# Kernel tuning notes

Measured on AMD Instinct MI355X. Metric: run time of the kernel, lower is better.

## Reference

```python
import math
import jax, jax.numpy as jnp
import numpy as np

N_HEAD = 16
STEP_DIM = 4


def _make_mask(T):
    # lower-triangular causal mask with every STEP_DIM-th column zeroed
    m = jnp.tril(jnp.ones((T, T), dtype=jnp.float32))
    cols = jnp.arange(T)
    keep_col = (cols % STEP_DIM) != (STEP_DIM - 1)
    return m * keep_col[None, :].astype(jnp.float32)  # [T, T]


def setup_inputs() -> dict:
    key = jax.random.key(0)
    ks = jax.random.split(key, 9)
    B, T, C = 2, 2048, 1024
    s = 1.0 / math.sqrt(C)
    return {
        "x": jax.random.normal(ks[0], (B, T, C), dtype=jnp.float32),
        "Wq": jax.random.normal(ks[1], (C, C), dtype=jnp.float32) * s,
        "bq": jnp.zeros((C,), dtype=jnp.float32),
        "Wk": jax.random.normal(ks[2], (C, C), dtype=jnp.float32) * s,
        "bk": jnp.zeros((C,), dtype=jnp.float32),
        "Wv": jax.random.normal(ks[3], (C, C), dtype=jnp.float32) * s,
        "bv": jnp.zeros((C,), dtype=jnp.float32),
        "Wp": jax.random.normal(ks[4], (C, C), dtype=jnp.float32) * s,
        "bp": jnp.zeros((C,), dtype=jnp.float32),
    }


def reference(x, Wq, bq, Wk, bk, Wv, bv, Wp, bp):
    B, T, C = x.shape
    H = N_HEAD
    D = C // H
    # QKV projections -> [B, H, T, D]
    def heads(y):
        return y.reshape(B, T, H, D).transpose(0, 2, 1, 3)
    q = heads(x @ Wq + bq)
    k = heads(x @ Wk + bk)
    v = heads(x @ Wv + bv)
    # scores [B, H, T, T]
    att = jnp.einsum("bhtd,bhsd->bhts", q, k) * (1.0 / math.sqrt(D))
    mask = _make_mask(T)  # [T, T]
    att = jnp.where(mask[None, None, :, :] == 0, -jnp.inf, att)
    att = jax.nn.softmax(att, axis=-1)
    y = jnp.einsum("bhts,bhsd->bhtd", att, v)  # [B, H, T, D]
    y = y.transpose(0, 2, 1, 3).reshape(B, T, C)
    return y @ Wp + bp
```

## Files before the change

kernel.cpp:

```cpp
#include <hip/hip_runtime.h>

typedef __bf16 bf16x8 __attribute__((ext_vector_type(8)));
typedef float  f32x4  __attribute__((ext_vector_type(4)));
typedef unsigned int u32x2 __attribute__((ext_vector_type(2)));
typedef __attribute__((address_space(3))) const unsigned short* lds_cp;

#define T_SEQ 2048
#define C_DIM 1024
#define NH    16
#define HD    64
#define LOG2E 1.4426950408889634f

__device__ __forceinline__ unsigned short f2bf(float f) {
  unsigned u = __builtin_bit_cast(unsigned, f);
  u += 0x7FFFu + ((u >> 16) & 1u);
  return (unsigned short)(u >> 16);
}

__device__ __forceinline__ unsigned cvtpk(float lo, float hi) {
  unsigned r;
  asm("v_cvt_pk_bf16_f32 %0, %1, %2" : "=v"(r) : "v"(lo), "v"(hi));
  return r;
}

__device__ __forceinline__ bf16x8 tr_frag(lds_cp addr) {
  u32x2 lo, hi;
  asm volatile("ds_read_b64_tr_b16 %0, %2 offset:0\n\t"
               "ds_read_b64_tr_b16 %1, %2 offset:128"
               : "=&v"(lo), "=&v"(hi) : "v"(addr) : "memory");
  struct { u32x2 a, b; } s{lo, hi};
  return __builtin_bit_cast(bf16x8, s);
}

__device__ __forceinline__ void gload_lds16(const void* g, void* l) {
  __builtin_amdgcn_global_load_lds(
      (const __attribute__((address_space(1))) unsigned int*)g,
      (__attribute__((address_space(3))) unsigned int*)l, 16, 0, 0);
}

__global__ void k_cvt_x(const float* __restrict__ x, unsigned short* __restrict__ xb) {
  const int i = blockIdx.x * 256 + threadIdx.x;
  const float4 v = ((const float4*)x)[i];
  ushort4 o;
  o.x = f2bf(v.x); o.y = f2bf(v.y); o.z = f2bf(v.z); o.w = f2bf(v.w);
  ((ushort4*)xb)[i] = o;
}

__global__ void k_transpose_w(const float* __restrict__ W, unsigned short* __restrict__ Wt) {
  __shared__ float tile[32][33];
  const int tx = threadIdx.x, ty = threadIdx.y;
  const int n0 = blockIdx.x * 32, k0 = blockIdx.y * 32;
#pragma unroll
  for (int i = 0; i < 32; i += 8)
    tile[ty + i][tx] = W[(size_t)(k0 + ty + i) * C_DIM + n0 + tx];
  __syncthreads();
#pragma unroll
  for (int i = 0; i < 32; i += 8)
    Wt[(size_t)(n0 + ty + i) * C_DIM + k0 + tx] = f2bf(tile[tx][ty + i]);
}

__global__ void k_concat_bias(const float* __restrict__ bq, const float* __restrict__ bk,
                              const float* __restrict__ bv, float* __restrict__ o) {
  const int i = blockIdx.x * 256 + threadIdx.x;
  o[i] = (i < 1024) ? bq[i] : (i < 2048 ? bk[i - 1024] : bv[i - 2048]);
}

template<int KDIM>
__device__ __forceinline__ void gemm_tile_mainloop(
    const unsigned short* __restrict__ A,
    const unsigned short* __restrict__ Bt,
    int m0, int n0,
    unsigned short* As, unsigned short* Bs,
    f32x4 acc[4][4])
{
  const int tid  = threadIdx.x;
  const int lane = tid & 63;
  const int wave = tid >> 6;
  const int wr   = wave >> 1, wc = wave & 1;
  const int srow = lane >> 2;
  const int scol = (lane & 3) << 3;
  const int fr   = lane & 15, g = lane >> 4;

  const f32x4 zero = {0.f, 0.f, 0.f, 0.f};
#pragma unroll
  for (int m = 0; m < 4; ++m)
#pragma unroll
    for (int n = 0; n < 4; ++n) acc[m][n] = zero;

  const int nk = KDIM >> 5;
  for (int kt = 0; kt < nk; ++kt) {
    const int kb = kt << 5;
#pragma unroll
    for (int i = 0; i < 2; ++i) {
      const int c   = wave * 2 + i;
      const int row = c * 16 + srow;
      gload_lds16(A  + (size_t)(m0 + row) * KDIM + kb + scol, As + c * 512);
      gload_lds16(Bt + (size_t)(n0 + row) * KDIM + kb + scol, Bs + c * 512);
    }
    __syncthreads();
    bf16x8 af[4], bfr[4];
    const unsigned short* ap = As + (wr * 64 + fr) * 32 + g * 8;
    const unsigned short* bp = Bs + (wc * 64 + fr) * 32 + g * 8;
#pragma unroll
    for (int m = 0; m < 4; ++m) af[m]  = *(const bf16x8*)(ap + m * 512);
#pragma unroll
    for (int n = 0; n < 4; ++n) bfr[n] = *(const bf16x8*)(bp + n * 512);
#pragma unroll
    for (int m = 0; m < 4; ++m)
#pragma unroll
      for (int n = 0; n < 4; ++n)
        acc[m][n] = __builtin_amdgcn_mfma_f32_16x16x32_bf16(af[m], bfr[n], acc[m][n], 0, 0, 0);
    __syncthreads();
  }
}

__global__ __launch_bounds__(256) void k_gemm_qkv(
    const unsigned short* __restrict__ Xb,
    const unsigned short* __restrict__ Wt,
    const float* __restrict__ bias,
    unsigned short* __restrict__ Qb,
    unsigned short* __restrict__ Kb,
    unsigned short* __restrict__ Vt)
{
  __shared__ __attribute__((aligned(16))) unsigned short As[128 * 32];
  __shared__ __attribute__((aligned(16))) unsigned short Bs[128 * 32];
  f32x4 acc[4][4];
  const int m0 = blockIdx.y * 128, n0 = blockIdx.x * 128;
  gemm_tile_mainloop<1024>(Xb, Wt, m0, n0, As, Bs, acc);

  const int lane = threadIdx.x & 63, wave = threadIdx.x >> 6;
  const int wr = wave >> 1, wc = wave & 1;
  const int fr = lane & 15, g = lane >> 4;
  const int j = n0 >> 10;
#pragma unroll
  for (int ni = 0; ni < 4; ++ni) {
    const int col = n0 + wc * 64 + ni * 16 + fr;
    const int c = col & 1023, h = c >> 6, d = c & 63;
    const float bb = bias[col];
#pragma unroll
    for (int mi = 0; mi < 4; ++mi)
#pragma unroll
      for (int r = 0; r < 4; ++r) {
        const int row = m0 + wr * 64 + mi * 16 + g * 4 + r;
        const int b = row >> 11, t = row & 2047;
        const int bh = b * NH + h;
        const float v = acc[mi][ni][r] + bb;
        if (j == 0)      Qb[((size_t)bh * T_SEQ + t) * HD + d] = f2bf(v * (0.125f * LOG2E));
        else if (j == 1) Kb[((size_t)bh * T_SEQ + t) * HD + d] = f2bf(v);
        else             Vt[((size_t)bh * HD + d) * T_SEQ + t] = f2bf(v);
      }
  }
}

__global__ __launch_bounds__(128) void k_attn(
    const unsigned short* __restrict__ Qb,
    const unsigned short* __restrict__ Kb,
    const unsigned short* __restrict__ Vt,
    unsigned short* __restrict__ Yb)
{
  __shared__ __attribute__((aligned(128))) unsigned short Ks[2][64][64];
  __shared__ __attribute__((aligned(128))) unsigned short Vs[2][64][64];
  __shared__ __attribute__((aligned(128))) unsigned short Pc[2][2][64][16];

  const int i    = blockIdx.x;
  const int xcd  = i & 7;
  const int jj   = i >> 3;
  const int bh   = xcd * 4 + (jj & 3);
  const int qtile = 31 - (jj >> 2);
  const int lane  = threadIdx.x & 63;
  const int wave  = threadIdx.x >> 6;
  const int fr = lane & 15, g = lane >> 4;
  const int q0w = qtile * 64 + wave * 32;
  const int nt = qtile + 1;
  const size_t hbase = (size_t)bh * T_SEQ * HD;
  const unsigned short* Kh = Kb + hbase;
  const unsigned short* Vh = Vt + (size_t)bh * HD * T_SEQ;

  const int srow = lane >> 3;
  const int scol = ((lane & 7) ^ srow) << 3;
  const int frx  = (fr & 7) << 3;

  const unsigned short* qp = Qb + hbase + (size_t)(q0w + fr) * HD + g * 8;
  const bf16x8 qA0 = *(const bf16x8*)(qp);
  const bf16x8 qA1 = *(const bf16x8*)(qp + 32);
  const bf16x8 qB0 = *(const bf16x8*)(qp + 16 * HD);
  const bf16x8 qB1 = *(const bf16x8*)(qp + 16 * HD + 32);

  const f32x4 zero = {0.f, 0.f, 0.f, 0.f};
  f32x4 yA[4], yB[4];
#pragma unroll
  for (int n = 0; n < 4; ++n) { yA[n] = zero; yB[n] = zero; }
  float lA[4], lB[4];
#pragma unroll
  for (int r = 0; r < 4; ++r) { lA[r] = 0.f; lB[r] = 0.f; }
  const float colmul = ((fr & 3) != 3) ? 1.0f : 0.0f;

  char* pwA = (char*)&Pc[wave][0][0][0] + fr * 32 + g * 8;
  char* pwB = (char*)&Pc[wave][1][0][0] + fr * 32 + g * 8;
  lds_cp trA = (lds_cp)(const unsigned short*)&Pc[wave][0][0][0] + fr * 4 + g * 128;
  lds_cp trB = (lds_cp)(const unsigned short*)&Pc[wave][1][0][0] + fr * 4 + g * 128;

  auto STAGE = [&](int buf, int s0) {
#pragma unroll
    for (int i2 = 0; i2 < 4; ++i2) {
      const int c = wave * 4 + i2;
      gload_lds16(Kh + (size_t)(s0 + c * 8 + srow) * HD + scol, &Ks[buf][c * 8][0]);
      gload_lds16(Vh + (size_t)(c * 8 + srow) * T_SEQ + s0 + scol, &Vs[buf][c * 8][0]);
    }
  };

  auto BODY = [&](int cur, int s0, bool diag) {
    bf16x8 kf[4][2];
#pragma unroll
    for (int n = 0; n < 4; ++n) {
      const unsigned short* kr = &Ks[cur][n * 16 + fr][0];
      kf[n][0] = *(const bf16x8*)(kr + ((g * 8) ^ frx));
      kf[n][1] = *(const bf16x8*)(kr + ((32 + g * 8) ^ frx));
    }
    f32x4 sA[4], sB[4];
#pragma unroll
    for (int n = 0; n < 4; ++n) {
      f32x4 a = zero, b = zero;
      a = __builtin_amdgcn_mfma_f32_16x16x32_bf16(qA0, kf[n][0], a, 0, 0, 0);
      a = __builtin_amdgcn_mfma_f32_16x16x32_bf16(qA1, kf[n][1], a, 0, 0, 0);
      b = __builtin_amdgcn_mfma_f32_16x16x32_bf16(qB0, kf[n][0], b, 0, 0, 0);
      b = __builtin_amdgcn_mfma_f32_16x16x32_bf16(qB1, kf[n][1], b, 0, 0, 0);
      sA[n] = a; sB[n] = b;
    }
    if (diag) {
      const bool colok = (fr & 3) != 3;
#pragma unroll
      for (int n = 0; n < 4; ++n) {
        const int sc = s0 + n * 16 + fr;
#pragma unroll
        for (int r = 0; r < 4; ++r) {
          const int tA = q0w + g * 4 + r;
          sA[n][r] = (colok && sc <= tA) ? sA[n][r] : -1e30f;
          sB[n][r] = (colok && sc <= tA + 16) ? sB[n][r] : -1e30f;
        }
      }
    }
    bf16x8 vf[4][2];
#pragma unroll
    for (int n = 0; n < 4; ++n) {
      const unsigned short* vr = &Vs[cur][n * 16 + fr][0];
      vf[n][0] = *(const bf16x8*)(vr + ((g * 8) ^ frx));
      vf[n][1] = *(const bf16x8*)(vr + ((32 + g * 8) ^ frx));
    }
#pragma unroll
    for (int n = 0; n < 4; ++n) {
      float pa0 = exp2f(sA[n][0]), pa1 = exp2f(sA[n][1]);
      float pa2 = exp2f(sA[n][2]), pa3 = exp2f(sA[n][3]);
      float pb0 = exp2f(sB[n][0]), pb1 = exp2f(sB[n][1]);
      float pb2 = exp2f(sB[n][2]), pb3 = exp2f(sB[n][3]);
      if (!diag) {
        pa0 *= colmul; pa1 *= colmul; pa2 *= colmul; pa3 *= colmul;
        pb0 *= colmul; pb1 *= colmul; pb2 *= colmul; pb3 *= colmul;
      }
      lA[0] += pa0; lA[1] += pa1; lA[2] += pa2; lA[3] += pa3;
      lB[0] += pb0; lB[1] += pb1; lB[2] += pb2; lB[3] += pb3;
      u32x2 wa = {cvtpk(pa0, pa1), cvtpk(pa2, pa3)};
      u32x2 wb = {cvtpk(pb0, pb1), cvtpk(pb2, pb3)};
      *(u32x2*)(pwA + n * 512) = wa;
      *(u32x2*)(pwB + n * 512) = wb;
    }
    bf16x8 paA[2], paB[2];
    paA[0] = tr_frag(trA);       paA[1] = tr_frag(trA + 512);
    paB[0] = tr_frag(trB);       paB[1] = tr_frag(trB + 512);
    asm volatile("s_waitcnt lgkmcnt(0)" ::: "memory");
    __builtin_amdgcn_sched_barrier(0);
#pragma unroll
    for (int kk = 0; kk < 2; ++kk)
#pragma unroll
      for (int n = 0; n < 4; ++n) {
        yA[n] = __builtin_amdgcn_mfma_f32_16x16x32_bf16(paA[kk], vf[n][kk], yA[n], 0, 0, 0);
        yB[n] = __builtin_amdgcn_mfma_f32_16x16x32_bf16(paB[kk], vf[n][kk], yB[n], 0, 0, 0);
      }
  };

  STAGE(0, 0);
  __syncthreads();
  for (int t = 0; t < nt; ++t) {
    const int cur = t & 1;
    if (t + 1 < nt) STAGE(cur ^ 1, (t + 1) * 64);
    const int s0 = t * 64;
    BODY(cur, s0, s0 + 63 > q0w);
    __syncthreads();
  }

#pragma unroll
  for (int off = 1; off < 16; off <<= 1)
#pragma unroll
    for (int r = 0; r < 4; ++r) {
      lA[r] += __shfl_xor(lA[r], off, 64);
      lB[r] += __shfl_xor(lB[r], off, 64);
    }
  const int b = bh >> 4, h = bh & 15;
#pragma unroll
  for (int r = 0; r < 4; ++r) {
    const float invA = 1.0f / lA[r], invB = 1.0f / lB[r];
    const int tA = q0w + g * 4 + r;
#pragma unroll
    for (int n = 0; n < 4; ++n) {
      Yb[((size_t)(b * T_SEQ + tA)) * C_DIM + h * HD + n * 16 + fr] = f2bf(yA[n][r] * invA);
      Yb[((size_t)(b * T_SEQ + tA + 16)) * C_DIM + h * HD + n * 16 + fr] = f2bf(yB[n][r] * invB);
    }
  }
}

__global__ __launch_bounds__(256) void k_gemm_out(
    const unsigned short* __restrict__ Yb,
    const unsigned short* __restrict__ Wpt,
    const float* __restrict__ bp,
    float* __restrict__ out)
{
  __shared__ __attribute__((aligned(16))) unsigned short As[128 * 32];
  __shared__ __attribute__((aligned(16))) unsigned short Bs[128 * 32];
  f32x4 acc[4][4];
  const int m0 = blockIdx.y * 128, n0 = blockIdx.x * 128;
  gemm_tile_mainloop<1024>(Yb, Wpt, m0, n0, As, Bs, acc);

  const int lane = threadIdx.x & 63, wave = threadIdx.x >> 6;
  const int wr = wave >> 1, wc = wave & 1;
  const int fr = lane & 15, g = lane >> 4;
#pragma unroll
  for (int ni = 0; ni < 4; ++ni) {
    const int col = n0 + wc * 64 + ni * 16 + fr;
    const float bb = bp[col];
#pragma unroll
    for (int mi = 0; mi < 4; ++mi)
#pragma unroll
      for (int r = 0; r < 4; ++r) {
        const int row = m0 + wr * 64 + mi * 16 + g * 4 + r;
        out[(size_t)row * C_DIM + col] = acc[mi][ni][r] + bb;
      }
  }
}

extern "C" void kernel_launch(void* const* d_in, const int* in_sizes, int n_in,
                              void* d_out, int out_size, void* d_ws, size_t ws_size,
                              hipStream_t stream) {
  const float* x  = (const float*)d_in[0];
  const float* Wq = (const float*)d_in[1];
  const float* bq = (const float*)d_in[2];
  const float* Wk = (const float*)d_in[3];
  const float* bk = (const float*)d_in[4];
  const float* Wv = (const float*)d_in[5];
  const float* bv = (const float*)d_in[6];
  const float* Wp = (const float*)d_in[7];
  const float* bp = (const float*)d_in[8];
  float* out = (float*)d_out;

  char* ws = (char*)d_ws;
  unsigned short* Xb   = (unsigned short*)(ws);
  unsigned short* Wt   = (unsigned short*)(ws + (8u  << 20));
  unsigned short* Wpt  = (unsigned short*)(ws + (14u << 20));
  float*          bqkv = (float*)         (ws + (16u << 20));
  unsigned short* Qb   = (unsigned short*)(ws + (16u << 20) + (64u << 10));
  unsigned short* Kb   = (unsigned short*)(ws + (24u << 20) + (64u << 10));
  unsigned short* Vt   = (unsigned short*)(ws + (32u << 20) + (64u << 10));
  unsigned short* Yb   = (unsigned short*)(ws + (40u << 20) + (64u << 10));

  k_cvt_x<<<4096, 256, 0, stream>>>(x, Xb);
  dim3 tb(32, 8);
  k_transpose_w<<<dim3(32, 32), tb, 0, stream>>>(Wq, Wt);
  k_transpose_w<<<dim3(32, 32), tb, 0, stream>>>(Wk, Wt + (1u << 20));
  k_transpose_w<<<dim3(32, 32), tb, 0, stream>>>(Wv, Wt + (2u << 20));
  k_transpose_w<<<dim3(32, 32), tb, 0, stream>>>(Wp, Wpt);
  k_concat_bias<<<12, 256, 0, stream>>>(bq, bk, bv, bqkv);
  k_gemm_qkv<<<dim3(24, 32), 256, 0, stream>>>(Xb, Wt, bqkv, Qb, Kb, Vt);
  k_attn<<<dim3(1024), 128, 0, stream>>>(Qb, Kb, Vt, Yb);
  k_gemm_out<<<dim3(8, 32), 256, 0, stream>>>(Yb, Wpt, bp, out);
}
```

Measured before the change: 144.1 us.

## Fold column mask into V and compute softmax denominators via MFMA ones

The every-fourth-column mask is moved into the QKV projection by writing zeros into those V^T entries. Softmax row sums are computed by an extra MFMA against a bf16 vector of ones that has zeros in the masked positions, replacing per-element fp32 adds and the cross-lane shuffle reduction. This removes VALU work from the attention inner loop at the cost of two more MFMAs per k-step. The row sum now comes from bf16-rounded probabilities, which changes numerics slightly.

```diff
diff --git a/kernel.cpp b/kernel.cpp
--- a/kernel.cpp
+++ b/kernel.cpp
@@ -3,6 +3,7 @@
 typedef __bf16 bf16x8 __attribute__((ext_vector_type(8)));
 typedef float  f32x4  __attribute__((ext_vector_type(4)));
 typedef unsigned int u32x2 __attribute__((ext_vector_type(2)));
+typedef unsigned short u16x8 __attribute__((ext_vector_type(8)));
 typedef __attribute__((address_space(3))) const unsigned short* lds_cp;
 
 #define T_SEQ 2048
@@ -147,7 +148,8 @@
         const float v = acc[mi][ni][r] + bb;
         if (j == 0)      Qb[((size_t)bh * T_SEQ + t) * HD + d] = f2bf(v * (0.125f * LOG2E));
         else if (j == 1) Kb[((size_t)bh * T_SEQ + t) * HD + d] = f2bf(v);
-        else             Vt[((size_t)bh * HD + d) * T_SEQ + t] = f2bf(v);
+        else             Vt[((size_t)bh * HD + d) * T_SEQ + t] =
+                           ((t & 3) == 3) ? (unsigned short)0 : f2bf(v);
       }
   }
 }
@@ -186,14 +188,14 @@
   const bf16x8 qB0 = *(const bf16x8*)(qp + 16 * HD);
   const bf16x8 qB1 = *(const bf16x8*)(qp + 16 * HD + 32);
 
+  const u16x8 bo = {0x3F80u, 0x3F80u, 0x3F80u, 0u, 0x3F80u, 0x3F80u, 0x3F80u, 0u};
+  const bf16x8 bones = __builtin_bit_cast(bf16x8, bo);
+
   const f32x4 zero = {0.f, 0.f, 0.f, 0.f};
-  f32x4 yA[4], yB[4];
+  f32x4 yA[4], yB[4], lAcc, lBcc;
 #pragma unroll
   for (int n = 0; n < 4; ++n) { yA[n] = zero; yB[n] = zero; }
-  float lA[4], lB[4];
-#pragma unroll
-  for (int r = 0; r < 4; ++r) { lA[r] = 0.f; lB[r] = 0.f; }
-  const float colmul = ((fr & 3) != 3) ? 1.0f : 0.0f;
+  lAcc = zero; lBcc = zero;
 
   char* pwA = (char*)&Pc[wave][0][0][0] + fr * 32 + g * 8;
   char* pwB = (char*)&Pc[wave][1][0][0] + fr * 32 + g * 8;
@@ -228,15 +230,14 @@
       sA[n] = a; sB[n] = b;
     }
     if (diag) {
-      const bool colok = (fr & 3) != 3;
 #pragma unroll
       for (int n = 0; n < 4; ++n) {
         const int sc = s0 + n * 16 + fr;
 #pragma unroll
         for (int r = 0; r < 4; ++r) {
           const int tA = q0w + g * 4 + r;
-          sA[n][r] = (colok && sc <= tA) ? sA[n][r] : -1e30f;
-          sB[n][r] = (colok && sc <= tA + 16) ? sB[n][r] : -1e30f;
+          sA[n][r] = (sc <= tA) ? sA[n][r] : -1e30f;
+          sB[n][r] = (sc <= tA + 16) ? sB[n][r] : -1e30f;
         }
       }
     }
@@ -249,18 +250,10 @@
     }
 #pragma unroll
     for (int n = 0; n < 4; ++n) {
-      float pa0 = exp2f(sA[n][0]), pa1 = exp2f(sA[n][1]);
-      float pa2 = exp2f(sA[n][2]), pa3 = exp2f(sA[n][3]);
-      float pb0 = exp2f(sB[n][0]), pb1 = exp2f(sB[n][1]);
-      float pb2 = exp2f(sB[n][2]), pb3 = exp2f(sB[n][3]);
-      if (!diag) {
-        pa0 *= colmul; pa1 *= colmul; pa2 *= colmul; pa3 *= colmul;
-        pb0 *= colmul; pb1 *= colmul; pb2 *= colmul; pb3 *= colmul;
-      }
-      lA[0] += pa0; lA[1] += pa1; lA[2] += pa2; lA[3] += pa3;
-      lB[0] += pb0; lB[1] += pb1; lB[2] += pb2; lB[3] += pb3;
-      u32x2 wa = {cvtpk(pa0, pa1), cvtpk(pa2, pa3)};
-      u32x2 wb = {cvtpk(pb0, pb1), cvtpk(pb2, pb3)};
+      u32x2 wa = {cvtpk(exp2f(sA[n][0]), exp2f(sA[n][1])),
+                  cvtpk(exp2f(sA[n][2]), exp2f(sA[n][3]))};
+      u32x2 wb = {cvtpk(exp2f(sB[n][0]), exp2f(sB[n][1])),
+                  cvtpk(exp2f(sB[n][2]), exp2f(sB[n][3]))};
       *(u32x2*)(pwA + n * 512) = wa;
       *(u32x2*)(pwB + n * 512) = wb;
     }
@@ -270,12 +263,15 @@
     asm volatile("s_waitcnt lgkmcnt(0)" ::: "memory");
     __builtin_amdgcn_sched_barrier(0);
 #pragma unroll
-    for (int kk = 0; kk < 2; ++kk)
+    for (int kk = 0; kk < 2; ++kk) {
 #pragma unroll
       for (int n = 0; n < 4; ++n) {
         yA[n] = __builtin_amdgcn_mfma_f32_16x16x32_bf16(paA[kk], vf[n][kk], yA[n], 0, 0, 0);
         yB[n] = __builtin_amdgcn_mfma_f32_16x16x32_bf16(paB[kk], vf[n][kk], yB[n], 0, 0, 0);
       }
+      lAcc = __builtin_amdgcn_mfma_f32_16x16x32_bf16(paA[kk], bones, lAcc, 0, 0, 0);
+      lBcc = __builtin_amdgcn_mfma_f32_16x16x32_bf16(paB[kk], bones, lBcc, 0, 0, 0);
+    }
   };
 
   STAGE(0, 0);
@@ -288,17 +284,10 @@
     __syncthreads();
   }
 
-#pragma unroll
-  for (int off = 1; off < 16; off <<= 1)
-#pragma unroll
-    for (int r = 0; r < 4; ++r) {
-      lA[r] += __shfl_xor(lA[r], off, 64);
-      lB[r] += __shfl_xor(lB[r], off, 64);
-    }
   const int b = bh >> 4, h = bh & 15;
 #pragma unroll
   for (int r = 0; r < 4; ++r) {
-    const float invA = 1.0f / lA[r], invB = 1.0f / lB[r];
+    const float invA = 1.0f / lAcc[r], invB = 1.0f / lBcc[r];
     const int tA = q0w + g * 4 + r;
 #pragma unroll
     for (int n = 0; n < 4; ++n) {
```

New measurement: 144.6 us. Within noise of the previous version (+0.3%).
